# Kernel optimization log

Hardware: AMD Instinct MI355X
Metric: run time of the kernel (lower is better)

The kernel has to match this reference:

```python
import jax, jax.numpy as jnp
import numpy as np

B, L, H, LAT, V = 4096, 16, 256, 64, 800


def setup_inputs() -> dict:
    key = jax.random.key(0)
    ks = jax.random.split(key, 20)
    s = 0.05
    return {
        'wid': jax.random.randint(ks[0], (B, L), 0, V),
        'tree_vec': jax.random.normal(ks[1], (B, LAT), jnp.float32),
        'emb': jax.random.normal(ks[2], (V, H), jnp.float32) * s,
        'Wz_w': jax.random.normal(ks[3], (H, 2 * H), jnp.float32) * s,
        'Wz_b': jnp.zeros((H,), jnp.float32),
        'Wr_w': jax.random.normal(ks[4], (H, H), jnp.float32) * s,
        'Ur_w': jax.random.normal(ks[5], (H, H), jnp.float32) * s,
        'Ur_b': jnp.zeros((H,), jnp.float32),
        'Wh_w': jax.random.normal(ks[6], (H, 2 * H), jnp.float32) * s,
        'Wh_b': jnp.zeros((H,), jnp.float32),
        'W_w': jax.random.normal(ks[7], (H, LAT + H), jnp.float32) * s,
        'W_b': jnp.zeros((H,), jnp.float32),
        'U_w': jax.random.normal(ks[8], (H, LAT + 2 * H), jnp.float32) * s,
        'U_b': jnp.zeros((H,), jnp.float32),
        'Wo_w': jax.random.normal(ks[9], (V, H), jnp.float32) * s,
        'Wo_b': jnp.zeros((V,), jnp.float32),
        'Us_w': jax.random.normal(ks[10], (1, H), jnp.float32) * s,
        'Us_b': jnp.zeros((1,), jnp.float32),
    }


def _decoder(wid, tree_vec, emb, Wz_w, Wz_b, Wr_w, Ur_w, Ur_b, Wh_w, Wh_b,
             W_w, W_b, U_w, U_b, Wo_w, Wo_b, Us_w, Us_b):
    nB, nL = wid.shape
    x = emb[wid]                      # [B,L,H] node embeddings
    xt = jnp.transpose(x, (1, 0, 2))  # [L,B,H]

    def gru_scan(src_seq, dst_seq):
        # JTNN GRUUpdate along a chain: carry = (m_prev, rm_prev)
        def step(carry, xs):
            m_prev, rm_prev = carry
            x_src, x_dst = xs
            z = jax.nn.sigmoid(jnp.concatenate([x_src, m_prev], -1) @ Wz_w.T + Wz_b)
            h_til = jnp.tanh(jnp.concatenate([x_src, rm_prev], -1) @ Wh_w.T + Wh_b)
            m = (1.0 - z) * m_prev + z * h_til
            r = jax.nn.sigmoid(x_dst @ Wr_w.T + m @ Ur_w.T + Ur_b)
            return (m, r * m), m
        z0 = jnp.zeros((src_seq.shape[1], H), src_seq.dtype)
        _, m_seq = jax.lax.scan(step, (z0, z0), (src_seq, dst_seq))
        return m_seq  # [L-1,B,H]

    # forward edges t->t+1 (DFS forward), reverse edges t+1->t (DFS backtrack)
    m_fwd = gru_scan(xt[:-1], xt[1:])
    m_rev = gru_scan(xt[1:][::-1], xt[:-1][::-1])[::-1]  # indexed by t

    zeros_h = jnp.zeros((nB, H), x.dtype)
    tvL = lambda n: jnp.broadcast_to(tree_vec, (n, nB, LAT))

    # p_inputs = [x_v, h_v, tree_vec] at root, each fwd step, each rev step
    p_root = jnp.concatenate([x[:, 0], zeros_h, tree_vec], -1)[None]
    p_fwd = jnp.concatenate([xt[1:], m_fwd, tvL(nL - 1)], -1)
    m_fwd_shift = jnp.concatenate([zeros_h[None], m_fwd[:-1]], 0)
    h_rev = m_fwd_shift + m_rev  # node t after backtrack pull
    p_rev = jnp.concatenate([xt[:-1], h_rev, tvL(nL - 1)], -1)[::-1]
    p_in = jnp.concatenate([p_root, p_fwd, p_rev], 0).reshape(-1, 2 * H + LAT)
    # targets: forward expansions -> 1, backtracks + final stop -> 0
    p_t = jnp.concatenate([jnp.ones((nL - 1,)), jnp.zeros((nL,))])
    p_t = jnp.broadcast_to(p_t[:, None], (2 * nL - 1, nB)).reshape(-1)

    # q_inputs = [h, tree_vec] at root and each newly created node
    q_root = jnp.concatenate([zeros_h, tree_vec], -1)[None]
    q_new = jnp.concatenate([m_fwd, tvL(nL - 1)], -1)
    q_in = jnp.concatenate([q_root, q_new], 0).reshape(-1, H + LAT)
    q_t = jnp.transpose(wid, (1, 0)).reshape(-1)  # [L*B], step-major like q_in

    q = jax.nn.relu(q_in @ W_w.T + W_b) @ Wo_w.T + Wo_b  # [L*B, V]
    p = (jax.nn.relu(p_in @ U_w.T + U_b) @ Us_w.T + Us_b)[:, 0]

    p_loss = jnp.sum(jnp.logaddexp(0.0, p) - p * p_t) / nB
    logZ = jax.nn.logsumexp(q, axis=-1)
    q_sel = jnp.take_along_axis(q, q_t[:, None], axis=1)[:, 0]
    q_loss = jnp.sum(logZ - q_sel) / nB
    p_acc = jnp.mean(((p > 0).astype(jnp.int32) == p_t.astype(jnp.int32)).astype(jnp.float32))
    q_acc = jnp.mean((jnp.argmax(q, axis=-1) == q_t).astype(jnp.float32))
    return (q_loss, p_loss, q_acc, p_acc)


def reference(wid, tree_vec, emb, Wz_w, Wz_b, Wr_w, Ur_w, Ur_b, Wh_w, Wh_b,
              W_w, W_b, U_w, U_b, Wo_w, Wo_b, Us_w, Us_b):
    return _decoder(wid, tree_vec, emb, Wz_w, Wz_b, Wr_w, Ur_w, Ur_b, Wh_w, Wh_b,
                    W_w, W_b, U_w, U_b, Wo_w, Wo_b, Us_w, Us_b)
```

## Files before the change

kernel.cpp:

```cpp
#include <hip/hip_runtime.h>
#include <math.h>


typedef unsigned short u16;
typedef __attribute__((ext_vector_type(4))) float f4;
typedef __attribute__((ext_vector_type(4))) unsigned short u16x4;
typedef __attribute__((ext_vector_type(8))) unsigned short u16x8;
typedef __attribute__((ext_vector_type(8))) short s16x8;
typedef __attribute__((ext_vector_type(4))) float f32x4;

#define DEV static __device__ __forceinline__

DEV u16 f2b(float f) {
  unsigned u = __float_as_uint(f);
  u += 0x7fffu + ((u >> 16) & 1u);
  return (u16)(u >> 16);
}
DEV float b2f(u16 h) { return __uint_as_float(((unsigned)h) << 16); }
DEV void split2(float v, u16& hi, u16& lo) {
  hi = f2b(v);
  lo = f2b(v - b2f(hi));
}
DEV float fsig(float x) { return __builtin_amdgcn_rcpf(1.f + __expf(-x)); }
DEV float ftanh(float x) {
  const float e = __expf(2.f * x);
  return 1.f - 2.f * __builtin_amdgcn_rcpf(e + 1.f);
}

DEV void gld16(const void* g, void* l) {
  __builtin_amdgcn_global_load_lds((const __attribute__((address_space(1))) void*)g,
                                   (__attribute__((address_space(3))) void*)l, 16, 0, 0);
}

#define MFMA(a, b, c) __builtin_amdgcn_mfma_f32_16x16x32_bf16((a), (b), (c), 0, 0, 0)

template <int GR, int GC, bool ASPL, bool BSPL>
DEV void mm128(const u16* __restrict__ Ah, const u16* __restrict__ Al,
               const u16* __restrict__ Bh, const u16* __restrict__ Bl,
               int K, u16* sm, f32x4* acc) {
  constexpr int MT = 8 / GR, NT = 8 / GC;
  const int tid = threadIdx.x;
  const int lane = tid & 63;
  const int wv = tid >> 6;
  const int wr = wv / GC, wc = wv % GC;
  const size_t rs = (size_t)K * 2;
  const size_t soff = (size_t)(tid >> 2) * rs + (size_t)((tid & 3) * 16);
  const char* gAh = (const char*)Ah + soff;
  const char* gBh = (const char*)Bh + soff;
  const char* gAl = nullptr;
  const char* gBl = nullptr;
  if constexpr (ASPL) gAl = (const char*)Al + soff;
  if constexpr (BSPL) gBl = (const char*)Bl + soff;
  char* L = (char*)sm;
  const int wb = wv * 1024;
  const int frow = lane & 15, fkb = (lane >> 4) * 16;
  const char* rA = L + (size_t)((wr * 16 * MT + frow) * 64 + fkb);
  const char* rB = L + 8192 + (size_t)((wc * 16 * NT + frow) * 64 + fkb);
  const size_t rskip = rs * 64;
  const int nk = K >> 5;
  for (int kt = 0; kt < nk; ++kt) {
    gld16(gAh, L + wb);
    gld16(gAh + rskip, L + 4096 + wb);
    gld16(gBh, L + 8192 + wb);
    gld16(gBh + rskip, L + 12288 + wb);
    if constexpr (ASPL) {
      gld16(gAl, L + 16384 + wb);
      gld16(gAl + rskip, L + 20480 + wb);
    }
    if constexpr (BSPL) {
      gld16(gBl, L + 24576 + wb);
      gld16(gBl + rskip, L + 28672 + wb);
    }
    gAh += 64; gBh += 64;
    if constexpr (ASPL) gAl += 64;
    if constexpr (BSPL) gBl += 64;
    __syncthreads();
    s16x8 a_[MT], b_[NT];
#pragma unroll
    for (int i = 0; i < MT; ++i) a_[i] = *(const s16x8*)(rA + i * 1024);
#pragma unroll
    for (int j = 0; j < NT; ++j) b_[j] = *(const s16x8*)(rB + j * 1024);
#pragma unroll
    for (int i = 0; i < MT; ++i)
#pragma unroll
      for (int j = 0; j < NT; ++j)
        acc[i * NT + j] = MFMA(a_[i], b_[j], acc[i * NT + j]);
    if constexpr (BSPL) {
      s16x8 bl_[NT];
#pragma unroll
      for (int j = 0; j < NT; ++j) bl_[j] = *(const s16x8*)(rB + 16384 + j * 1024);
#pragma unroll
      for (int i = 0; i < MT; ++i)
#pragma unroll
        for (int j = 0; j < NT; ++j)
          acc[i * NT + j] = MFMA(a_[i], bl_[j], acc[i * NT + j]);
    }
    if constexpr (ASPL) {
      s16x8 al_[MT];
#pragma unroll
      for (int i = 0; i < MT; ++i) al_[i] = *(const s16x8*)(rA + 16384 + i * 1024);
#pragma unroll
      for (int i = 0; i < MT; ++i)
#pragma unroll
        for (int j = 0; j < NT; ++j)
          acc[i * NT + j] = MFMA(al_[i], b_[j], acc[i * NT + j]);
    }
    __syncthreads();
  }
}

__global__ __launch_bounds__(256) void k_pack(const float* __restrict__ Wz, const float* __restrict__ Wr,
                                              const float* __restrict__ Ur, const float* __restrict__ Wh,
                                              const float* __restrict__ Ww, const float* __restrict__ Uw,
                                              const float* __restrict__ Wo, const float* __restrict__ emb,
                                              const float* __restrict__ tree,
                                              u16* wpk, u16* uzh, u16* urw, u16* wu, u16* wt2, u16* wov,
                                              u16* uxp2, u16* utp2, u16* embp, u16* tre2) {
  const int i = blockIdx.x * 256 + threadIdx.x;
  const int seg = blockIdx.y;
  u16 h, l;
  if (seg == 0) {
    if (i >= 196608) return;
    const int row = i >> 8, c = i & 255;
    const float v = (row < 256) ? Wz[row * 512 + c]
                                : (row < 512) ? Wh[(row - 256) * 512 + c] : Wr[(row - 512) * 256 + c];
    split2(v, h, l); wpk[i] = h; wpk[196608 + i] = l;
  } else if (seg == 1) {
    if (i >= 131072) return;
    const int row = i >> 8, c = i & 255;
    const float v = (row < 256) ? Wz[row * 512 + 256 + c] : Wh[(row - 256) * 512 + 256 + c];
    uzh[i] = f2b(v);
  } else if (seg == 2) {
    if (i >= 65536) return;
    urw[i] = f2b(Ur[i]);
  } else if (seg == 3) {
    if (i >= 81920) return;
    if (i < 65536) {
      const int row = i >> 8, c = i & 255;
      wu[i] = f2b(Ww[row * 320 + c]);
    } else {
      const int j = i - 65536, row = j >> 6, c = j & 63;
      split2(Ww[row * 320 + 256 + c], h, l); wt2[j] = h; wt2[16384 + j] = l;
    }
  } else if (seg == 4) {
    if (i >= 229376) return;
    const float v = (i < 204800) ? Wo[i] : 0.f;
    wov[i] = f2b(v);
  } else if (seg == 5) {
    if (i >= 147456) return;
    if (i < 65536) {
      const int row = i >> 8, c = i & 255;
      split2(Uw[row * 576 + c], h, l); uxp2[i] = h; uxp2[65536 + i] = l;
    } else if (i < 131072) {
      const int j = i - 65536, row = j >> 8, c = j & 255;
      wu[65536 + j] = f2b(Uw[row * 576 + 256 + c]);
    } else {
      const int j = i - 131072, row = j >> 6, c = j & 63;
      split2(Uw[row * 576 + 512 + c], h, l); utp2[j] = h; utp2[16384 + j] = l;
    }
  } else if (seg == 6) {
    if (i >= 229376) return;
    const int row = i >> 8;
    const float v = (row < 800) ? emb[i] : 0.f;
    split2(v, h, l); embp[i] = h; embp[229376 + i] = l;
  } else {
    if (i >= 65536) return;
    const int b = i >> 4, c4 = (i & 15) << 2;
    const f4 tv = *(const f4*)(tree + (size_t)b * 64 + c4);
    u16x4 hi, lo;
#pragma unroll
    for (int k = 0; k < 4; ++k) { u16 hh, ll; split2(tv[k], hh, ll); hi[k] = hh; lo[k] = ll; }
    *(u16x4*)(tre2 + (size_t)b * 64 + c4) = hi;
    *(u16x4*)(tre2 + 262144 + (size_t)b * 64 + c4) = lo;
  }
}

__global__ __launch_bounds__(256) void k_prep(const u16* __restrict__ embp, const u16* __restrict__ wpk,
                                              const u16* __restrict__ tre2, const u16* __restrict__ wt2,
                                              const u16* __restrict__ utp2, const u16* __restrict__ uxp2,
                                              u16* __restrict__ Aembh, float* __restrict__ Tq,
                                              float* __restrict__ Tp, float* __restrict__ Xp) {
  __shared__ u16 sm[16384];
  f32x4 acc[16] = {};
  const int bid = blockIdx.x;
  int seg, bx, by, K;
  const u16 *A0, *B0;
  size_t Aoff, Boff;
  if (bid < 42) { seg = 0; bx = bid % 7; by = bid / 7; A0 = embp; Aoff = 229376; B0 = wpk; Boff = 196608; K = 256; }
  else if (bid < 106) { const int l2 = bid - 42; seg = 1; bx = l2 % 32; by = l2 / 32; A0 = tre2; Aoff = 262144; B0 = wt2; Boff = 16384; K = 64; }
  else if (bid < 170) { const int l2 = bid - 106; seg = 2; bx = l2 % 32; by = l2 / 32; A0 = tre2; Aoff = 262144; B0 = utp2; Boff = 16384; K = 64; }
  else { const int l2 = bid - 170; seg = 3; bx = l2 % 7; by = l2 / 7; A0 = embp; Aoff = 229376; B0 = uxp2; Boff = 65536; K = 256; }
  A0 += (size_t)bx * 128 * K;
  B0 += (size_t)by * 128 * K;
  mm128<2, 2, true, true>(A0, A0 + Aoff, B0, B0 + Boff, K, sm, acc);
  const int lane = threadIdx.x & 63, wv = threadIdx.x >> 6;
  const int wr = wv >> 1, wc = wv & 1, quad = lane >> 4, c = lane & 15;
#pragma unroll
  for (int i = 0; i < 4; ++i)
#pragma unroll
    for (int j = 0; j < 4; ++j)
#pragma unroll
      for (int rg = 0; rg < 4; ++rg) {
        const size_t row = (size_t)bx * 128 + wr * 64 + i * 16 + quad * 4 + rg;
        const int col = by * 128 + wc * 64 + j * 16 + c;
        const float v = acc[i * 4 + j][rg];
        if (seg == 0) Aembh[row * 768 + col] = f2b(v);
        else if (seg == 1) Tq[row * 256 + col] = v;
        else if (seg == 2) Tp[row * 256 + col] = v;
        else Xp[row * 256 + col] = v;
      }
}

__global__ __launch_bounds__(1024, 1) void k_scan(const u16* __restrict__ uzh, const u16* __restrict__ urw,
                                                  const u16* __restrict__ Aembh, const int* __restrict__ wid,
                                                  const float* __restrict__ Wz_b, const float* __restrict__ Wh_b,
                                                  const float* __restrict__ Ur_b,
                                                  u16* __restrict__ mfh, u16* __restrict__ mrh) {
  __shared__ __align__(16) u16 MH[8192];
  __shared__ __align__(16) u16 ML[8192];
  __shared__ __align__(16) u16 RH[8192];
  __shared__ __align__(16) u16 RL[8192];
  const int tid = threadIdx.x;
  const int wv = tid >> 6, lane = tid & 63;
  const int l15 = lane & 15, quad = lane >> 4;
  const int r0 = blockIdx.x * 32;
  const int dir = r0 >> 12;
  const int b0 = r0 & 4095;
  for (int i = tid; i < 8192; i += 1024) { MH[i] = 0; ML[i] = 0; RH[i] = 0; RL[i] = 0; }
  const int zc0 = wv * 16;
  const int cc = zc0 + l15;
  const float bzv = Wz_b[cc], bhv = Wh_b[cc], urv = Ur_b[cc];
  s16x8 wz[8], wh[8];
#pragma unroll
  for (int kc = 0; kc < 8; ++kc) {
    const size_t zo = (size_t)cc * 256 + kc * 32 + quad * 8;
    wz[kc] = *(const s16x8*)(uzh + zo);
    wh[kc] = *(const s16x8*)(uzh + zo + 65536);
  }
  float mnew[2][4];
  __syncthreads();
  for (int s = 0; s < 15; ++s) {
    const int tsrc = dir ? (15 - s) : s;
    const int tdst = dir ? (14 - s) : (s + 1);
    int xids[8], xds[8];
#pragma unroll
    for (int mt = 0; mt < 2; ++mt)
#pragma unroll
      for (int rg = 0; rg < 4; ++rg) {
        const int b = b0 + mt * 16 + quad * 4 + rg;
        xids[mt * 4 + rg] = wid[b * 16 + tsrc];
        xds[mt * 4 + rg] = (s < 14) ? wid[b * 16 + tdst] : 0;
      }
    f32x4 aZ[2] = {};
    f32x4 aH[2] = {};
    for (int kc = 0; kc < 8; ++kc) {
      s16x8 amh[2], aml[2], arh[2], arl[2];
#pragma unroll
      for (int mt = 0; mt < 2; ++mt) {
        const int ai = ((kc * 4 + quad) * 32 + mt * 16 + l15) * 8;
        amh[mt] = *(const s16x8*)&MH[ai];
        aml[mt] = *(const s16x8*)&ML[ai];
        arh[mt] = *(const s16x8*)&RH[ai];
        arl[mt] = *(const s16x8*)&RL[ai];
      }
#pragma unroll
      for (int mt = 0; mt < 2; ++mt) {
        aZ[mt] = MFMA(amh[mt], wz[kc], aZ[mt]);
        aZ[mt] = MFMA(aml[mt], wz[kc], aZ[mt]);
        aH[mt] = MFMA(arh[mt], wh[kc], aH[mt]);
        aH[mt] = MFMA(arl[mt], wh[kc], aH[mt]);
      }
    }
    __syncthreads();
#pragma unroll
    for (int mt = 0; mt < 2; ++mt)
#pragma unroll
      for (int rg = 0; rg < 4; ++rg) {
        const int rr = mt * 16 + quad * 4 + rg;
        const int xid = xids[mt * 4 + rg];
        const int mi = ((cc >> 3) * 32 + rr) * 8 + (cc & 7);
        const float az = b2f(Aembh[(size_t)xid * 768 + cc]);
        const float ah = b2f(Aembh[(size_t)xid * 768 + 256 + cc]);
        const float mp = b2f(MH[mi]) + b2f(ML[mi]);
        const float z = fsig(aZ[mt][rg] + az + bzv);
        const float ht = ftanh(aH[mt][rg] + ah + bhv);
        const float mv = (1.f - z) * mp + z * ht;
        mnew[mt][rg] = mv;
        u16 hh, ll; split2(mv, hh, ll);
        MH[mi] = hh; ML[mi] = ll;
      }
    __syncthreads();
    {
      u16* dst = dir ? (mrh + ((size_t)(14 - s) * 4096 + b0) * 256)
                     : (mfh + ((size_t)s * 4096 + b0) * 256);
      const int r = tid >> 5, cg = tid & 31;
      const s16x8 v = *(const s16x8*)&MH[(cg * 32 + r) * 8];
      *(s16x8*)(dst + r * 256 + cg * 8) = v;
    }
    if (s == 14) break;
    f32x4 aR[2] = {};
    for (int kc = 0; kc < 8; ++kc) {
      s16x8 amh[2], aml[2];
#pragma unroll
      for (int mt = 0; mt < 2; ++mt) {
        const int ai = ((kc * 4 + quad) * 32 + mt * 16 + l15) * 8;
        amh[mt] = *(const s16x8*)&MH[ai];
        aml[mt] = *(const s16x8*)&ML[ai];
      }
      const size_t ro = (size_t)cc * 256 + kc * 32 + quad * 8;
      const s16x8 brh = *(const s16x8*)(urw + ro);
#pragma unroll
      for (int mt = 0; mt < 2; ++mt) {
        aR[mt] = MFMA(amh[mt], brh, aR[mt]);
        aR[mt] = MFMA(aml[mt], brh, aR[mt]);
      }
    }
#pragma unroll
    for (int mt = 0; mt < 2; ++mt)
#pragma unroll
      for (int rg = 0; rg < 4; ++rg) {
        const int rr = mt * 16 + quad * 4 + rg;
        const int xd = xds[mt * 4 + rg];
        const int mi = ((cc >> 3) * 32 + rr) * 8 + (cc & 7);
        const float ar = b2f(Aembh[(size_t)xd * 768 + 512 + cc]);
        const float rp = aR[mt][rg] + ar + urv;
        const float rmv = fsig(rp) * mnew[mt][rg];
        u16 hh, ll; split2(rmv, hh, ll);
        RH[mi] = hh; RL[mi] = ll;
      }
    __syncthreads();
  }
}

__global__ __launch_bounds__(256) void k_mid(const u16* __restrict__ mfh, const u16* __restrict__ mrh,
                                             const u16* __restrict__ wu,
                                             const float* __restrict__ Tq, const float* __restrict__ W_b,
                                             const float* __restrict__ Xp, const float* __restrict__ Tp,
                                             const float* __restrict__ U_b, const float* __restrict__ Us_w,
                                             const int* __restrict__ wid,
                                             u16* __restrict__ hq, u16* __restrict__ hrev,
                                             float* __restrict__ ppart) {
  const int bid = blockIdx.x;
  const int tid = threadIdx.x;
  if (bid < 1920) {
    __shared__ u16 sm[8192];
    f32x4 acc[16] = {};
    const int rb = bid >> 2, ct = bid & 3;
    const u16* Ah = mfh + (size_t)rb * 128 * 256;
    const u16* Bh = wu + (size_t)ct * 128 * 256;
    mm128<4, 1, false, false>(Ah, nullptr, Bh, nullptr, 256, sm, acc);
    const int lane = tid & 63, wv = tid >> 6, quad = lane >> 4, c = lane & 15;
    if (ct < 2) {
      const int colb = ct * 128;
#pragma unroll
      for (int i = 0; i < 2; ++i)
#pragma unroll
        for (int rg = 0; rg < 4; ++rg) {
          const size_t row = (size_t)rb * 128 + wv * 32 + i * 16 + quad * 4 + rg;
          const int b = (int)(row & 4095);
#pragma unroll
          for (int j = 0; j < 8; ++j) {
            const int col = colb + j * 16 + c;
            const float hv = fmaxf(acc[i * 8 + j][rg] + Tq[(size_t)b * 256 + col] + W_b[col], 0.f);
            hq[(row + 4096) * 256 + col] = f2b(hv);
          }
        }
    } else {
      const int colb = (ct - 2) * 128;
#pragma unroll
      for (int i = 0; i < 2; ++i)
#pragma unroll
        for (int rg = 0; rg < 4; ++rg) {
          const size_t row = (size_t)rb * 128 + wv * 32 + i * 16 + quad * 4 + rg;
          const int t = (int)(row >> 12), b = (int)(row & 4095);
          const int xid = wid[b * 16 + t + 1];
          const int prow = (int)row + 4096;
          float d = 0.f;
#pragma unroll
          for (int j = 0; j < 8; ++j) {
            const int col = colb + j * 16 + c;
            float h = acc[i * 8 + j][rg] + Xp[(size_t)xid * 256 + col] + Tp[(size_t)b * 256 + col] + U_b[col];
            h = fmaxf(h, 0.f);
            d += h * Us_w[col];
          }
#pragma unroll
          for (int dd = 1; dd < 16; dd <<= 1) d += __shfl_xor(d, dd);
          if (c == 0) ppart[(size_t)prow * 2 + (ct - 2)] = d;
        }
    }
  } else if (bid < 9600) {
    const int idx = (bid - 1920) * 256 + tid;
    const int r = idx >> 5, g8 = idx & 31;
    const int t = r >> 12;
    const size_t o = (size_t)r * 256 + g8 * 8;
    const u16x8 a = *(const u16x8*)(mrh + o);
    u16x8 out = a;
    if (t > 0) {
      const u16x8 a2 = *(const u16x8*)(mfh + o - 1048576);
#pragma unroll
      for (int k = 0; k < 8; ++k) out[k] = f2b(b2f(a[k]) + b2f(a2[k]));
    }
    *(u16x8*)(hrev + o) = out;
  } else {
    const int b = bid - 9600;
    const int col = tid;
    const float hv = fmaxf(Tq[(size_t)b * 256 + col] + W_b[col], 0.f);
    hq[(size_t)b * 256 + col] = f2b(hv);
    const int xid = wid[b * 16];
    float d = fmaxf(Xp[(size_t)xid * 256 + col] + Tp[(size_t)b * 256 + col] + U_b[col], 0.f) * Us_w[col];
#pragma unroll
    for (int dd = 1; dd < 64; dd <<= 1) d += __shfl_xor(d, dd);
    __shared__ float red[4];
    if ((tid & 63) == 0) red[tid >> 6] = d;
    __syncthreads();
    if (tid == 0) {
      ppart[(size_t)b * 2] = red[0] + red[1] + red[2] + red[3];
      ppart[(size_t)b * 2 + 1] = 0.f;
    }
  }
}

__global__ __launch_bounds__(256) void k_tail(const u16* __restrict__ hq, const u16* __restrict__ wov,
                                              const u16* __restrict__ wu, const u16* __restrict__ hrev,
                                              const float* __restrict__ Wo_b, const float* __restrict__ Xp,
                                              const float* __restrict__ Tp, const float* __restrict__ U_b,
                                              const float* __restrict__ Us_w, const int* __restrict__ wid,
                                              float* __restrict__ accb, float* __restrict__ ppart) {
  __shared__ __align__(16) u16 smem[40960];
  const int bid = blockIdx.x;
  const int tid = threadIdx.x, lane = tid & 63, wv = tid >> 6;
  const int quad = lane >> 4, c = lane & 15;
  if (bid < 512) {
    char* LA = (char*)smem;
    char* LB = (char*)(smem + 32768);
    const u16* Ah = hq + (size_t)bid * 128 * 256;
    const size_t soff = (size_t)(tid >> 2) * 512 + (size_t)((tid & 3) * 16);
#pragma unroll
    for (int kt = 0; kt < 8; ++kt) {
      gld16((const char*)Ah + soff + kt * 64, LA + kt * 8192 + wv * 1024);
      gld16((const char*)Ah + soff + 32768 + kt * 64, LA + kt * 8192 + 4096 + wv * 1024);
    }
    gld16((const char*)wov + soff, LB + wv * 1024);
    gld16((const char*)wov + soff + 32768, LB + 4096 + wv * 1024);
    float rM[8], rS[8], rSel[8];
    int rAm[8], qts[8];
#pragma unroll
    for (int mt = 0; mt < 2; ++mt)
#pragma unroll
      for (int rg = 0; rg < 4; ++rg) {
        const int r8 = mt * 4 + rg;
        rM[r8] = -1e30f; rS[r8] = 0.f; rSel[r8] = -1e30f; rAm[r8] = 0x7fffffff;
        const size_t row = (size_t)bid * 128 + wv * 32 + mt * 16 + quad * 4 + rg;
        qts[r8] = wid[(row & 4095) * 16 + (int)(row >> 12)];
      }
    f32x4 acc[16];
    for (int nt = 0; nt < 7; ++nt) {
#pragma unroll
      for (int i = 0; i < 16; ++i) acc[i] = (f32x4){0.f, 0.f, 0.f, 0.f};
      for (int kt = 0; kt < 8; ++kt) {
        const int g = nt * 8 + kt;
        __syncthreads();
        if (g < 55) {
          const int nn = (g + 1) >> 3, nk = (g + 1) & 7;
          const char* Bn = (const char*)(wov + (size_t)nn * 32768) + soff + nk * 64;
          gld16(Bn, LB + ((g + 1) & 1) * 8192 + wv * 1024);
          gld16(Bn + 32768, LB + ((g + 1) & 1) * 8192 + 4096 + wv * 1024);
        }
        s16x8 af[2], bf[8];
#pragma unroll
        for (int mt = 0; mt < 2; ++mt)
          af[mt] = *(const s16x8*)(LA + kt * 8192 + (wv * 32 + mt * 16 + c) * 64 + quad * 16);
#pragma unroll
        for (int j = 0; j < 8; ++j)
          bf[j] = *(const s16x8*)(LB + (g & 1) * 8192 + (j * 16 + c) * 64 + quad * 16);
#pragma unroll
        for (int mt = 0; mt < 2; ++mt)
#pragma unroll
          for (int j = 0; j < 8; ++j)
            acc[mt * 8 + j] = MFMA(af[mt], bf[j], acc[mt * 8 + j]);
      }
      const int colb = nt * 128;
#pragma unroll
      for (int mt = 0; mt < 2; ++mt)
#pragma unroll
        for (int rg = 0; rg < 4; ++rg) {
          const int r8 = mt * 4 + rg;
          float vals[8];
          float mx = -1e30f;
          int am = 0x7fffffff;
#pragma unroll
          for (int j = 0; j < 8; ++j) {
            const int col = colb + j * 16 + c;
            float v = -1e30f;
            if (col < 800) v = acc[mt * 8 + j][rg] + Wo_b[col];
            vals[j] = v;
            if (v > mx) { mx = v; am = col; }
          }
          float gm = mx;
          int ga = am;
#pragma unroll
          for (int d = 1; d < 16; d <<= 1) {
            const float om = __shfl_xor(gm, d);
            const int oa = __shfl_xor(ga, d);
            if (om > gm || (om == gm && oa < ga)) { gm = om; ga = oa; }
          }
          float s = 0.f, sel = -1e30f;
#pragma unroll
          for (int j = 0; j < 8; ++j) {
            s += __expf(vals[j] - gm);
            if (colb + j * 16 + c == qts[r8]) sel = vals[j];
          }
#pragma unroll
          for (int d = 1; d < 16; d <<= 1) {
            s += __shfl_xor(s, d);
            sel = fmaxf(sel, __shfl_xor(sel, d));
          }
          const float oM = rM[r8];
          if (gm > oM || (gm == oM && ga < rAm[r8])) rAm[r8] = ga;
          const float nM = fmaxf(oM, gm);
          rS[r8] = rS[r8] * __expf(oM - nM) + s * __expf(gm - nM);
          rM[r8] = nM;
          rSel[r8] = fmaxf(rSel[r8], sel);
        }
    }
    __syncthreads();
    float* qred = (float*)smem;
    if (tid == 0) { qred[0] = 0.f; qred[1] = 0.f; }
    __syncthreads();
    if (c == 0) {
      float lsum = 0.f, hsum = 0.f;
#pragma unroll
      for (int r8 = 0; r8 < 8; ++r8) {
        lsum += rM[r8] + logf(rS[r8]) - rSel[r8];
        hsum += (rAm[r8] == qts[r8]) ? 1.f : 0.f;
      }
      atomicAdd(&qred[0], lsum);
      atomicAdd(&qred[1], hsum);
    }
    __syncthreads();
    if (tid == 0) {
      atomicAdd(&accb[bid & 15], qred[0]);
      atomicAdd(&accb[16 + (bid & 15)], qred[1]);
    }
  } else {
    f32x4 acc[16] = {};
    const int l2 = bid - 512;
    const int by = l2 & 1, bx = l2 >> 1;
    const u16* Ah = hrev + (size_t)bx * 128 * 256;
    const u16* Bh = wu + (size_t)(256 + by * 128) * 256;
    mm128<4, 1, false, false>(Ah, nullptr, Bh, nullptr, 256, smem, acc);
    const int colb = by * 128;
#pragma unroll
    for (int i = 0; i < 2; ++i)
#pragma unroll
      for (int rg = 0; rg < 4; ++rg) {
        const size_t row = (size_t)bx * 128 + wv * 32 + i * 16 + quad * 4 + rg;
        const int t = (int)(row >> 12), b = (int)(row & 4095);
        const int xid = wid[b * 16 + t];
        const int prow = (30 - t) * 4096 + b;
        float d = 0.f;
#pragma unroll
        for (int j = 0; j < 8; ++j) {
          const int col = colb + j * 16 + c;
          float h = acc[i * 8 + j][rg] + Xp[(size_t)xid * 256 + col] + Tp[(size_t)b * 256 + col] + U_b[col];
          h = fmaxf(h, 0.f);
          d += h * Us_w[col];
        }
#pragma unroll
        for (int dd = 1; dd < 16; dd <<= 1) d += __shfl_xor(d, dd);
        if (c == 0) ppart[(size_t)prow * 2 + by] = d;
      }
  }
}

__global__ __launch_bounds__(256) void k_red(const float* __restrict__ ppart, const float* __restrict__ Us_b,
                                             float* __restrict__ accb) {
  __shared__ float s0, s1;
  if (threadIdx.x == 0) { s0 = 0.f; s1 = 0.f; }
  __syncthreads();
  const int r = blockIdx.x * 256 + threadIdx.x;
  const float p = ppart[(size_t)r * 2] + ppart[(size_t)r * 2 + 1] + Us_b[0];
  const int sidx = r >> 12;
  const float pt = (sidx < 15) ? 1.f : 0.f;
  const float loss = fmaxf(p, 0.f) + log1pf(expf(-fabsf(p))) - p * pt;
  const float hit = ((p > 0.f) == (pt > 0.5f)) ? 1.f : 0.f;
  atomicAdd(&s0, loss);
  atomicAdd(&s1, hit);
  __syncthreads();
  if (threadIdx.x == 0) {
    atomicAdd(&accb[32 + (blockIdx.x & 15)], s0);
    atomicAdd(&accb[48 + (blockIdx.x & 15)], s1);
  }
}

__global__ void k_finalize(const float* __restrict__ accb, float* __restrict__ out) {
  if (threadIdx.x == 0 && blockIdx.x == 0) {
    float ql = 0, qa = 0, pl = 0, pa = 0;
    for (int i = 0; i < 16; ++i) {
      ql += accb[i];
      qa += accb[16 + i];
      pl += accb[32 + i];
      pa += accb[48 + i];
    }
    out[0] = ql / 4096.f;
    out[1] = pl / 4096.f;
    out[2] = qa / 65536.f;
    out[3] = pa / 126976.f;
  }
}

__global__ void k_flag(float* __restrict__ out) {
  if (threadIdx.x < 4) out[threadIdx.x] = -12345.f;
}

extern "C" void kernel_launch(void* const* d_in, const int* in_sizes, int n_in,
                              void* d_out, int out_size, void* d_ws, size_t ws_size,
                              hipStream_t stream) {
  (void)in_sizes; (void)n_in; (void)out_size;
  const int* wid = (const int*)d_in[0];
  const float* tree = (const float*)d_in[1];
  const float* emb = (const float*)d_in[2];
  const float* Wz_w = (const float*)d_in[3];
  const float* Wz_b = (const float*)d_in[4];
  const float* Wr_w = (const float*)d_in[5];
  const float* Ur_w = (const float*)d_in[6];
  const float* Ur_b = (const float*)d_in[7];
  const float* Wh_w = (const float*)d_in[8];
  const float* Wh_b = (const float*)d_in[9];
  const float* W_w = (const float*)d_in[10];
  const float* W_b = (const float*)d_in[11];
  const float* U_w = (const float*)d_in[12];
  const float* U_b = (const float*)d_in[13];
  const float* Wo_w = (const float*)d_in[14];
  const float* Wo_b = (const float*)d_in[15];
  const float* Us_w = (const float*)d_in[16];
  const float* Us_b = (const float*)d_in[17];
  char* ws = (char*)d_ws;

  constexpr size_t NEED = 152273152ull;
  if (ws_size < NEED) {
    k_flag<<<1, 64, 0, stream>>>((float*)d_out);
    return;
  }

  u16* hq = (u16*)(ws + 0ull);
  u16* hrev = (u16*)(ws + 33554432ull);
  u16* mfh = (u16*)(ws + 65011712ull);
  u16* mrh = (u16*)(ws + 96468992ull);
  u16* Aembh = (u16*)(ws + 127926272ull);
  u16* embp = (u16*)(ws + 129302528ull);
  u16* wpk = (u16*)(ws + 130220032ull);
  u16* uzh = (u16*)(ws + 131006464ull);
  u16* urw = (u16*)(ws + 131268608ull);
  u16* wu = (u16*)(ws + 131399680ull);
  u16* wt2 = (u16*)(ws + 131661824ull);
  u16* wov = (u16*)(ws + 131727360ull);
  u16* uxp2 = (u16*)(ws + 132186112ull);
  u16* utp2 = (u16*)(ws + 132448256ull);
  u16* tre2 = (u16*)(ws + 132513792ull);
  float* Tq = (float*)(ws + 133562368ull);
  float* Tp = (float*)(ws + 137756672ull);
  float* Xp = (float*)(ws + 141950976ull);
  float* ppart = (float*)(ws + 151257088ull);
  float* accb = (float*)(ws + 152272896ull);

  hipMemsetAsync(accb, 0, 256, stream);

  k_pack<<<dim3(896, 8), 256, 0, stream>>>(Wz_w, Wr_w, Ur_w, Wh_w, W_w, U_w, Wo_w, emb, tree,
                                           wpk, uzh, urw, wu, wt2, wov, uxp2, utp2, embp, tre2);
  k_prep<<<184, 256, 0, stream>>>(embp, wpk, tre2, wt2, utp2, uxp2, Aembh, Tq, Tp, Xp);
  k_scan<<<256, 1024, 0, stream>>>(uzh, urw, Aembh, wid, Wz_b, Wh_b, Ur_b, mfh, mrh);
  k_mid<<<13696, 256, 0, stream>>>(mfh, mrh, wu, Tq, W_b, Xp, Tp, U_b, Us_w, wid, hq, hrev, ppart);
  k_tail<<<1472, 256, 0, stream>>>(hq, wov, wu, hrev, Wo_b, Xp, Tp, U_b, Us_w, wid, accb, ppart);
  k_red<<<496, 256, 0, stream>>>(ppart, Us_b, accb);
  k_finalize<<<1, 64, 0, stream>>>(accb, (float*)d_out);
}
```

Measured before the change: 571.5 us.

## Fuse hrev construction into reverse-edge GEMM and restructure mid/tail kernels

The separate elementwise pass that built hrev in global memory is removed. The reverse-edge GEMM blocks now compute mrh + shifted mfh directly into shared memory before running the U-projection, and each forward row block runs all four column tiles itself so the A tile is loaded only once. Root-node work moves into a standalone kernel launched before the scan, and k_tail now only does the vocab logsumexp GEMM. This cuts the global write and read of a roughly 30 MB intermediate plus repeated A-tile loads, at the cost of fewer, heavier blocks in k_midG (960 instead of 13696).

```diff
diff --git a/kernel.cpp b/kernel.cpp
--- a/kernel.cpp
+++ b/kernel.cpp
@@ -332,244 +332,306 @@
   }
 }
 
-__global__ __launch_bounds__(256) void k_mid(const u16* __restrict__ mfh, const u16* __restrict__ mrh,
-                                             const u16* __restrict__ wu,
-                                             const float* __restrict__ Tq, const float* __restrict__ W_b,
-                                             const float* __restrict__ Xp, const float* __restrict__ Tp,
-                                             const float* __restrict__ U_b, const float* __restrict__ Us_w,
-                                             const int* __restrict__ wid,
-                                             u16* __restrict__ hq, u16* __restrict__ hrev,
-                                             float* __restrict__ ppart) {
+__global__ __launch_bounds__(256) void k_root(const float* __restrict__ Tq, const float* __restrict__ W_b,
+                                              const float* __restrict__ Xp, const float* __restrict__ Tp,
+                                              const float* __restrict__ U_b, const float* __restrict__ Us_w,
+                                              const int* __restrict__ wid,
+                                              u16* __restrict__ hq, float* __restrict__ ppart) {
+  const int b = blockIdx.x;
+  const int tid = threadIdx.x;
+  const int col = tid;
+  const float hv = fmaxf(Tq[(size_t)b * 256 + col] + W_b[col], 0.f);
+  hq[(size_t)b * 256 + col] = f2b(hv);
+  const int xid = wid[b * 16];
+  float d = fmaxf(Xp[(size_t)xid * 256 + col] + Tp[(size_t)b * 256 + col] + U_b[col], 0.f) * Us_w[col];
+#pragma unroll
+  for (int dd = 1; dd < 64; dd <<= 1) d += __shfl_xor(d, dd);
+  __shared__ float red[4];
+  if ((tid & 63) == 0) red[tid >> 6] = d;
+  __syncthreads();
+  if (tid == 0) {
+    ppart[(size_t)b * 2] = red[0] + red[1] + red[2] + red[3];
+    ppart[(size_t)b * 2 + 1] = 0.f;
+  }
+}
+
+__global__ __launch_bounds__(256) void k_midG(const u16* __restrict__ mfh, const u16* __restrict__ mrh,
+                                              const u16* __restrict__ wu,
+                                              const float* __restrict__ Tq, const float* __restrict__ W_b,
+                                              const float* __restrict__ Xp, const float* __restrict__ Tp,
+                                              const float* __restrict__ U_b, const float* __restrict__ Us_w,
+                                              const int* __restrict__ wid,
+                                              u16* __restrict__ hq, float* __restrict__ ppart) {
+  __shared__ __align__(16) u16 smem[40960];
+  char* LA = (char*)smem;
+  char* LB = (char*)(smem + 32768);
   const int bid = blockIdx.x;
-  const int tid = threadIdx.x;
-  if (bid < 1920) {
-    __shared__ u16 sm[8192];
-    f32x4 acc[16] = {};
-    const int rb = bid >> 2, ct = bid & 3;
+  const int tid = threadIdx.x, lane = tid & 63, wv = tid >> 6;
+  const int quad = lane >> 4, c = lane & 15;
+  const size_t soff = (size_t)(tid >> 2) * 512 + (size_t)((tid & 3) * 16);
+  if (bid < 480) {
+    const int rb = bid;
     const u16* Ah = mfh + (size_t)rb * 128 * 256;
-    const u16* Bh = wu + (size_t)ct * 128 * 256;
-    mm128<4, 1, false, false>(Ah, nullptr, Bh, nullptr, 256, sm, acc);
-    const int lane = tid & 63, wv = tid >> 6, quad = lane >> 4, c = lane & 15;
-    if (ct < 2) {
-      const int colb = ct * 128;
-#pragma unroll
-      for (int i = 0; i < 2; ++i)
+#pragma unroll
+    for (int kt = 0; kt < 8; ++kt) {
+      gld16((const char*)Ah + soff + kt * 64, LA + kt * 8192 + wv * 1024);
+      gld16((const char*)Ah + soff + 32768 + kt * 64, LA + kt * 8192 + 4096 + wv * 1024);
+    }
+    gld16((const char*)wu + soff, LB + wv * 1024);
+    gld16((const char*)wu + soff + 32768, LB + 4096 + wv * 1024);
+    f32x4 acc[16];
+    for (int nt = 0; nt < 4; ++nt) {
+#pragma unroll
+      for (int i = 0; i < 16; ++i) acc[i] = (f32x4){0.f, 0.f, 0.f, 0.f};
+      for (int kt = 0; kt < 8; ++kt) {
+        const int g = nt * 8 + kt;
+        __syncthreads();
+        if (g < 31) {
+          const int nn = (g + 1) >> 3, nk = (g + 1) & 7;
+          const char* Bn = (const char*)(wu + (size_t)nn * 32768) + soff + nk * 64;
+          gld16(Bn, LB + ((g + 1) & 1) * 8192 + wv * 1024);
+          gld16(Bn + 32768, LB + ((g + 1) & 1) * 8192 + 4096 + wv * 1024);
+        }
+        s16x8 af[2], bf[8];
+#pragma unroll
+        for (int mt = 0; mt < 2; ++mt)
+          af[mt] = *(const s16x8*)(LA + kt * 8192 + (wv * 32 + mt * 16 + c) * 64 + quad * 16);
+#pragma unroll
+        for (int j = 0; j < 8; ++j)
+          bf[j] = *(const s16x8*)(LB + (g & 1) * 8192 + (j * 16 + c) * 64 + quad * 16);
+#pragma unroll
+        for (int mt = 0; mt < 2; ++mt)
+#pragma unroll
+          for (int j = 0; j < 8; ++j)
+            acc[mt * 8 + j] = MFMA(af[mt], bf[j], acc[mt * 8 + j]);
+      }
+      if (nt < 2) {
+        const int colb = nt * 128;
+#pragma unroll
+        for (int mt = 0; mt < 2; ++mt)
+#pragma unroll
+          for (int rg = 0; rg < 4; ++rg) {
+            const size_t row = (size_t)rb * 128 + wv * 32 + mt * 16 + quad * 4 + rg;
+            const int b = (int)(row & 4095);
+#pragma unroll
+            for (int j = 0; j < 8; ++j) {
+              const int col = colb + j * 16 + c;
+              const float hv = fmaxf(acc[mt * 8 + j][rg] + Tq[(size_t)b * 256 + col] + W_b[col], 0.f);
+              hq[(row + 4096) * 256 + col] = f2b(hv);
+            }
+          }
+      } else {
+        const int colb = (nt - 2) * 128;
+#pragma unroll
+        for (int mt = 0; mt < 2; ++mt)
+#pragma unroll
+          for (int rg = 0; rg < 4; ++rg) {
+            const size_t row = (size_t)rb * 128 + wv * 32 + mt * 16 + quad * 4 + rg;
+            const int t = (int)(row >> 12), b = (int)(row & 4095);
+            const int xid = wid[b * 16 + t + 1];
+            const int prow = (int)row + 4096;
+            float d = 0.f;
+#pragma unroll
+            for (int j = 0; j < 8; ++j) {
+              const int col = colb + j * 16 + c;
+              float h = acc[mt * 8 + j][rg] + Xp[(size_t)xid * 256 + col] + Tp[(size_t)b * 256 + col] + U_b[col];
+              h = fmaxf(h, 0.f);
+              d += h * Us_w[col];
+            }
+#pragma unroll
+            for (int dd = 1; dd < 16; dd <<= 1) d += __shfl_xor(d, dd);
+            if (c == 0) ppart[(size_t)prow * 2 + (nt - 2)] = d;
+          }
+      }
+    }
+  } else {
+    const int bx = bid - 480;
+    for (int it = 0; it < 16; ++it) {
+      const int ch = it * 256 + tid;
+      const int gr = ch >> 5, oc = (ch & 31) * 8;
+      const int grow = bx * 128 + gr;
+      const int t = grow >> 12;
+      const size_t go = (size_t)grow * 256 + oc;
+      const u16x8 a = *(const u16x8*)(mrh + go);
+      u16x8 out = a;
+      if (t > 0) {
+        const u16x8 a2 = *(const u16x8*)(mfh + go - 1048576);
+#pragma unroll
+        for (int k = 0; k < 8; ++k) out[k] = f2b(b2f(a[k]) + b2f(a2[k]));
+      }
+      *(u16x8*)(LA + (oc >> 5) * 8192 + gr * 64 + (oc & 31) * 2) = out;
+    }
+    const u16* Bb = wu + 65536;
+    gld16((const char*)Bb + soff, LB + wv * 1024);
+    gld16((const char*)Bb + soff + 32768, LB + 4096 + wv * 1024);
+    f32x4 acc[16];
+    for (int nt = 0; nt < 2; ++nt) {
+#pragma unroll
+      for (int i = 0; i < 16; ++i) acc[i] = (f32x4){0.f, 0.f, 0.f, 0.f};
+      for (int kt = 0; kt < 8; ++kt) {
+        const int g = nt * 8 + kt;
+        __syncthreads();
+        if (g < 15) {
+          const int nn = (g + 1) >> 3, nk = (g + 1) & 7;
+          const char* Bn = (const char*)(Bb + (size_t)nn * 32768) + soff + nk * 64;
+          gld16(Bn, LB + ((g + 1) & 1) * 8192 + wv * 1024);
+          gld16(Bn + 32768, LB + ((g + 1) & 1) * 8192 + 4096 + wv * 1024);
+        }
+        s16x8 af[2], bf[8];
+#pragma unroll
+        for (int mt = 0; mt < 2; ++mt)
+          af[mt] = *(const s16x8*)(LA + kt * 8192 + (wv * 32 + mt * 16 + c) * 64 + quad * 16);
+#pragma unroll
+        for (int j = 0; j < 8; ++j)
+          bf[j] = *(const s16x8*)(LB + (g & 1) * 8192 + (j * 16 + c) * 64 + quad * 16);
+#pragma unroll
+        for (int mt = 0; mt < 2; ++mt)
+#pragma unroll
+          for (int j = 0; j < 8; ++j)
+            acc[mt * 8 + j] = MFMA(af[mt], bf[j], acc[mt * 8 + j]);
+      }
+      const int colb = nt * 128;
+#pragma unroll
+      for (int mt = 0; mt < 2; ++mt)
 #pragma unroll
         for (int rg = 0; rg < 4; ++rg) {
-          const size_t row = (size_t)rb * 128 + wv * 32 + i * 16 + quad * 4 + rg;
-          const int b = (int)(row & 4095);
+          const size_t row = (size_t)bx * 128 + wv * 32 + mt * 16 + quad * 4 + rg;
+          const int t = (int)(row >> 12), b = (int)(row & 4095);
+          const int xid = wid[b * 16 + t];
+          const int prow = (30 - t) * 4096 + b;
+          float d = 0.f;
 #pragma unroll
           for (int j = 0; j < 8; ++j) {
             const int col = colb + j * 16 + c;
-            const float hv = fmaxf(acc[i * 8 + j][rg] + Tq[(size_t)b * 256 + col] + W_b[col], 0.f);
-            hq[(row + 4096) * 256 + col] = f2b(hv);
-          }
-        }
-    } else {
-      const int colb = (ct - 2) * 128;
-#pragma unroll
-      for (int i = 0; i < 2; ++i)
-#pragma unroll
-        for (int rg = 0; rg < 4; ++rg) {
-          const size_t row = (size_t)rb * 128 + wv * 32 + i * 16 + quad * 4 + rg;
-          const int t = (int)(row >> 12), b = (int)(row & 4095);
-          const int xid = wid[b * 16 + t + 1];
-          const int prow = (int)row + 4096;
-          float d = 0.f;
-#pragma unroll
-          for (int j = 0; j < 8; ++j) {
-            const int col = colb + j * 16 + c;
-            float h = acc[i * 8 + j][rg] + Xp[(size_t)xid * 256 + col] + Tp[(size_t)b * 256 + col] + U_b[col];
+            float h = acc[mt * 8 + j][rg] + Xp[(size_t)xid * 256 + col] + Tp[(size_t)b * 256 + col] + U_b[col];
             h = fmaxf(h, 0.f);
             d += h * Us_w[col];
           }
 #pragma unroll
           for (int dd = 1; dd < 16; dd <<= 1) d += __shfl_xor(d, dd);
-          if (c == 0) ppart[(size_t)prow * 2 + (ct - 2)] = d;
+          if (c == 0) ppart[(size_t)prow * 2 + nt] = d;
         }
     }
-  } else if (bid < 9600) {
-    const int idx = (bid - 1920) * 256 + tid;
-    const int r = idx >> 5, g8 = idx & 31;
-    const int t = r >> 12;
-    const size_t o = (size_t)r * 256 + g8 * 8;
-    const u16x8 a = *(const u16x8*)(mrh + o);
-    u16x8 out = a;
-    if (t > 0) {
-      const u16x8 a2 = *(const u16x8*)(mfh + o - 1048576);
-#pragma unroll
-      for (int k = 0; k < 8; ++k) out[k] = f2b(b2f(a[k]) + b2f(a2[k]));
-    }
-    *(u16x8*)(hrev + o) = out;
-  } else {
-    const int b = bid - 9600;
-    const int col = tid;
-    const float hv = fmaxf(Tq[(size_t)b * 256 + col] + W_b[col], 0.f);
-    hq[(size_t)b * 256 + col] = f2b(hv);
-    const int xid = wid[b * 16];
-    float d = fmaxf(Xp[(size_t)xid * 256 + col] + Tp[(size_t)b * 256 + col] + U_b[col], 0.f) * Us_w[col];
-#pragma unroll
-    for (int dd = 1; dd < 64; dd <<= 1) d += __shfl_xor(d, dd);
-    __shared__ float red[4];
-    if ((tid & 63) == 0) red[tid >> 6] = d;
-    __syncthreads();
-    if (tid == 0) {
-      ppart[(size_t)b * 2] = red[0] + red[1] + red[2] + red[3];
-      ppart[(size_t)b * 2 + 1] = 0.f;
-    }
   }
 }
 
 __global__ __launch_bounds__(256) void k_tail(const u16* __restrict__ hq, const u16* __restrict__ wov,
-                                              const u16* __restrict__ wu, const u16* __restrict__ hrev,
-                                              const float* __restrict__ Wo_b, const float* __restrict__ Xp,
-                                              const float* __restrict__ Tp, const float* __restrict__ U_b,
-                                              const float* __restrict__ Us_w, const int* __restrict__ wid,
-                                              float* __restrict__ accb, float* __restrict__ ppart) {
+                                              const float* __restrict__ Wo_b, const int* __restrict__ wid,
+                                              float* __restrict__ accb) {
   __shared__ __align__(16) u16 smem[40960];
   const int bid = blockIdx.x;
   const int tid = threadIdx.x, lane = tid & 63, wv = tid >> 6;
   const int quad = lane >> 4, c = lane & 15;
-  if (bid < 512) {
-    char* LA = (char*)smem;
-    char* LB = (char*)(smem + 32768);
-    const u16* Ah = hq + (size_t)bid * 128 * 256;
-    const size_t soff = (size_t)(tid >> 2) * 512 + (size_t)((tid & 3) * 16);
-#pragma unroll
+  char* LA = (char*)smem;
+  char* LB = (char*)(smem + 32768);
+  const u16* Ah = hq + (size_t)bid * 128 * 256;
+  const size_t soff = (size_t)(tid >> 2) * 512 + (size_t)((tid & 3) * 16);
+#pragma unroll
+  for (int kt = 0; kt < 8; ++kt) {
+    gld16((const char*)Ah + soff + kt * 64, LA + kt * 8192 + wv * 1024);
+    gld16((const char*)Ah + soff + 32768 + kt * 64, LA + kt * 8192 + 4096 + wv * 1024);
+  }
+  gld16((const char*)wov + soff, LB + wv * 1024);
+  gld16((const char*)wov + soff + 32768, LB + 4096 + wv * 1024);
+  float rM[8], rS[8], rSel[8];
+  int rAm[8], qts[8];
+#pragma unroll
+  for (int mt = 0; mt < 2; ++mt)
+#pragma unroll
+    for (int rg = 0; rg < 4; ++rg) {
+      const int r8 = mt * 4 + rg;
+      rM[r8] = -1e30f; rS[r8] = 0.f; rSel[r8] = -1e30f; rAm[r8] = 0x7fffffff;
+      const size_t row = (size_t)bid * 128 + wv * 32 + mt * 16 + quad * 4 + rg;
+      qts[r8] = wid[(row & 4095) * 16 + (int)(row >> 12)];
+    }
+  f32x4 acc[16];
+  for (int nt = 0; nt < 7; ++nt) {
+#pragma unroll
+    for (int i = 0; i < 16; ++i) acc[i] = (f32x4){0.f, 0.f, 0.f, 0.f};
     for (int kt = 0; kt < 8; ++kt) {
-      gld16((const char*)Ah + soff + kt * 64, LA + kt * 8192 + wv * 1024);
-      gld16((const char*)Ah + soff + 32768 + kt * 64, LA + kt * 8192 + 4096 + wv * 1024);
-    }
-    gld16((const char*)wov + soff, LB + wv * 1024);
-    gld16((const char*)wov + soff + 32768, LB + 4096 + wv * 1024);
-    float rM[8], rS[8], rSel[8];
-    int rAm[8], qts[8];
+      const int g = nt * 8 + kt;
+      __syncthreads();
+      if (g < 55) {
+        const int nn = (g + 1) >> 3, nk = (g + 1) & 7;
+        const char* Bn = (const char*)(wov + (size_t)nn * 32768) + soff + nk * 64;
+        gld16(Bn, LB + ((g + 1) & 1) * 8192 + wv * 1024);
+        gld16(Bn + 32768, LB + ((g + 1) & 1) * 8192 + 4096 + wv * 1024);
+      }
+      s16x8 af[2], bf[8];
+#pragma unroll
+      for (int mt = 0; mt < 2; ++mt)
+        af[mt] = *(const s16x8*)(LA + kt * 8192 + (wv * 32 + mt * 16 + c) * 64 + quad * 16);
+#pragma unroll
+      for (int j = 0; j < 8; ++j)
+        bf[j] = *(const s16x8*)(LB + (g & 1) * 8192 + (j * 16 + c) * 64 + quad * 16);
+#pragma unroll
+      for (int mt = 0; mt < 2; ++mt)
+#pragma unroll
+        for (int j = 0; j < 8; ++j)
+          acc[mt * 8 + j] = MFMA(af[mt], bf[j], acc[mt * 8 + j]);
+    }
+    const int colb = nt * 128;
 #pragma unroll
     for (int mt = 0; mt < 2; ++mt)
 #pragma unroll
       for (int rg = 0; rg < 4; ++rg) {
         const int r8 = mt * 4 + rg;
-        rM[r8] = -1e30f; rS[r8] = 0.f; rSel[r8] = -1e30f; rAm[r8] = 0x7fffffff;
-        const size_t row = (size_t)bid * 128 + wv * 32 + mt * 16 + quad * 4 + rg;
-        qts[r8] = wid[(row & 4095) * 16 + (int)(row >> 12)];
-      }
-    f32x4 acc[16];
-    for (int nt = 0; nt < 7; ++nt) {
-#pragma unroll
-      for (int i = 0; i < 16; ++i) acc[i] = (f32x4){0.f, 0.f, 0.f, 0.f};
-      for (int kt = 0; kt < 8; ++kt) {
-        const int g = nt * 8 + kt;
-        __syncthreads();
-        if (g < 55) {
-          const int nn = (g + 1) >> 3, nk = (g + 1) & 7;
-          const char* Bn = (const char*)(wov + (size_t)nn * 32768) + soff + nk * 64;
-          gld16(Bn, LB + ((g + 1) & 1) * 8192 + wv * 1024);
-          gld16(Bn + 32768, LB + ((g + 1) & 1) * 8192 + 4096 + wv * 1024);
-        }
-        s16x8 af[2], bf[8];
-#pragma unroll
-        for (int mt = 0; mt < 2; ++mt)
-          af[mt] = *(const s16x8*)(LA + kt * 8192 + (wv * 32 + mt * 16 + c) * 64 + quad * 16);
-#pragma unroll
-        for (int j = 0; j < 8; ++j)
-          bf[j] = *(const s16x8*)(LB + (g & 1) * 8192 + (j * 16 + c) * 64 + quad * 16);
-#pragma unroll
-        for (int mt = 0; mt < 2; ++mt)
-#pragma unroll
-          for (int j = 0; j < 8; ++j)
-            acc[mt * 8 + j] = MFMA(af[mt], bf[j], acc[mt * 8 + j]);
-      }
-      const int colb = nt * 128;
-#pragma unroll
-      for (int mt = 0; mt < 2; ++mt)
-#pragma unroll
-        for (int rg = 0; rg < 4; ++rg) {
-          const int r8 = mt * 4 + rg;
-          float vals[8];
-          float mx = -1e30f;
-          int am = 0x7fffffff;
-#pragma unroll
-          for (int j = 0; j < 8; ++j) {
-            const int col = colb + j * 16 + c;
-            float v = -1e30f;
-            if (col < 800) v = acc[mt * 8 + j][rg] + Wo_b[col];
-            vals[j] = v;
-            if (v > mx) { mx = v; am = col; }
-          }
-          float gm = mx;
-          int ga = am;
-#pragma unroll
-          for (int d = 1; d < 16; d <<= 1) {
-            const float om = __shfl_xor(gm, d);
-            const int oa = __shfl_xor(ga, d);
-            if (om > gm || (om == gm && oa < ga)) { gm = om; ga = oa; }
-          }
-          float s = 0.f, sel = -1e30f;
-#pragma unroll
-          for (int j = 0; j < 8; ++j) {
-            s += __expf(vals[j] - gm);
-            if (colb + j * 16 + c == qts[r8]) sel = vals[j];
-          }
-#pragma unroll
-          for (int d = 1; d < 16; d <<= 1) {
-            s += __shfl_xor(s, d);
-            sel = fmaxf(sel, __shfl_xor(sel, d));
-          }
-          const float oM = rM[r8];
-          if (gm > oM || (gm == oM && ga < rAm[r8])) rAm[r8] = ga;
-          const float nM = fmaxf(oM, gm);
-          rS[r8] = rS[r8] * __expf(oM - nM) + s * __expf(gm - nM);
-          rM[r8] = nM;
-          rSel[r8] = fmaxf(rSel[r8], sel);
-        }
-    }
-    __syncthreads();
-    float* qred = (float*)smem;
-    if (tid == 0) { qred[0] = 0.f; qred[1] = 0.f; }
-    __syncthreads();
-    if (c == 0) {
-      float lsum = 0.f, hsum = 0.f;
-#pragma unroll
-      for (int r8 = 0; r8 < 8; ++r8) {
-        lsum += rM[r8] + logf(rS[r8]) - rSel[r8];
-        hsum += (rAm[r8] == qts[r8]) ? 1.f : 0.f;
-      }
-      atomicAdd(&qred[0], lsum);
-      atomicAdd(&qred[1], hsum);
-    }
-    __syncthreads();
-    if (tid == 0) {
-      atomicAdd(&accb[bid & 15], qred[0]);
-      atomicAdd(&accb[16 + (bid & 15)], qred[1]);
-    }
-  } else {
-    f32x4 acc[16] = {};
-    const int l2 = bid - 512;
-    const int by = l2 & 1, bx = l2 >> 1;
-    const u16* Ah = hrev + (size_t)bx * 128 * 256;
-    const u16* Bh = wu + (size_t)(256 + by * 128) * 256;
-    mm128<4, 1, false, false>(Ah, nullptr, Bh, nullptr, 256, smem, acc);
-    const int colb = by * 128;
-#pragma unroll
-    for (int i = 0; i < 2; ++i)
-#pragma unroll
-      for (int rg = 0; rg < 4; ++rg) {
-        const size_t row = (size_t)bx * 128 + wv * 32 + i * 16 + quad * 4 + rg;
-        const int t = (int)(row >> 12), b = (int)(row & 4095);
-        const int xid = wid[b * 16 + t];
-        const int prow = (30 - t) * 4096 + b;
-        float d = 0.f;
+        float vals[8];
+        float mx = -1e30f;
+        int am = 0x7fffffff;
 #pragma unroll
         for (int j = 0; j < 8; ++j) {
           const int col = colb + j * 16 + c;
-          float h = acc[i * 8 + j][rg] + Xp[(size_t)xid * 256 + col] + Tp[(size_t)b * 256 + col] + U_b[col];
-          h = fmaxf(h, 0.f);
-          d += h * Us_w[col];
+          float v = -1e30f;
+          if (col < 800) v = acc[mt * 8 + j][rg] + Wo_b[col];
+          vals[j] = v;
+          if (v > mx) { mx = v; am = col; }
         }
-#pragma unroll
-        for (int dd = 1; dd < 16; dd <<= 1) d += __shfl_xor(d, dd);
-        if (c == 0) ppart[(size_t)prow * 2 + by] = d;
-      }
+        float gm = mx;
+        int ga = am;
+#pragma unroll
+        for (int d = 1; d < 16; d <<= 1) {
+          const float om = __shfl_xor(gm, d);
+          const int oa = __shfl_xor(ga, d);
+          if (om > gm || (om == gm && oa < ga)) { gm = om; ga = oa; }
+        }
+        float s = 0.f, sel = -1e30f;
+#pragma unroll
+        for (int j = 0; j < 8; ++j) {
+          s += __expf(vals[j] - gm);
+          if (colb + j * 16 + c == qts[r8]) sel = vals[j];
+        }
+#pragma unroll
+        for (int d = 1; d < 16; d <<= 1) {
+          s += __shfl_xor(s, d);
+          sel = fmaxf(sel, __shfl_xor(sel, d));
+        }
+        const float oM = rM[r8];
+        if (gm > oM || (gm == oM && ga < rAm[r8])) rAm[r8] = ga;
+        const float nM = fmaxf(oM, gm);
+        rS[r8] = rS[r8] * __expf(oM - nM) + s * __expf(gm - nM);
+        rM[r8] = nM;
+        rSel[r8] = fmaxf(rSel[r8], sel);
+      }
+  }
+  __syncthreads();
+  float* qred = (float*)smem;
+  if (tid == 0) { qred[0] = 0.f; qred[1] = 0.f; }
+  __syncthreads();
+  if (c == 0) {
+    float lsum = 0.f, hsum = 0.f;
+#pragma unroll
+    for (int r8 = 0; r8 < 8; ++r8) {
+      lsum += rM[r8] + logf(rS[r8]) - rSel[r8];
+      hsum += (rAm[r8] == qts[r8]) ? 1.f : 0.f;
+    }
+    atomicAdd(&qred[0], lsum);
+    atomicAdd(&qred[1], hsum);
+  }
+  __syncthreads();
+  if (tid == 0) {
+    atomicAdd(&accb[bid & 15], qred[0]);
+    atomicAdd(&accb[16 + (bid & 15)], qred[1]);
   }
 }
 
@@ -644,7 +706,6 @@
   }
 
   u16* hq = (u16*)(ws + 0ull);
-  u16* hrev = (u16*)(ws + 33554432ull);
   u16* mfh = (u16*)(ws + 65011712ull);
   u16* mrh = (u16*)(ws + 96468992ull);
   u16* Aembh = (u16*)(ws + 127926272ull);
@@ -669,9 +730,10 @@
   k_pack<<<dim3(896, 8), 256, 0, stream>>>(Wz_w, Wr_w, Ur_w, Wh_w, W_w, U_w, Wo_w, emb, tree,
                                            wpk, uzh, urw, wu, wt2, wov, uxp2, utp2, embp, tre2);
   k_prep<<<184, 256, 0, stream>>>(embp, wpk, tre2, wt2, utp2, uxp2, Aembh, Tq, Tp, Xp);
+  k_root<<<4096, 256, 0, stream>>>(Tq, W_b, Xp, Tp, U_b, Us_w, wid, hq, ppart);
   k_scan<<<256, 1024, 0, stream>>>(uzh, urw, Aembh, wid, Wz_b, Wh_b, Ur_b, mfh, mrh);
-  k_mid<<<13696, 256, 0, stream>>>(mfh, mrh, wu, Tq, W_b, Xp, Tp, U_b, Us_w, wid, hq, hrev, ppart);
-  k_tail<<<1472, 256, 0, stream>>>(hq, wov, wu, hrev, Wo_b, Xp, Tp, U_b, Us_w, wid, accb, ppart);
+  k_midG<<<960, 256, 0, stream>>>(mfh, mrh, wu, Tq, W_b, Xp, Tp, U_b, Us_w, wid, hq, ppart);
+  k_tail<<<512, 256, 0, stream>>>(hq, wov, Wo_b, wid, accb);
   k_red<<<496, 256, 0, stream>>>(ppart, Us_b, accb);
   k_finalize<<<1, 64, 0, stream>>>(accb, (float*)d_out);
 }
```

Result: no change. 580.6 us (+1.6%).
